# Kernel optimization log

Measured on AMD Instinct MI355X. Metric: run time of the kernel, lower is better.

The kernel has to match this reference:

```python
import jax, jax.numpy as jnp
import numpy as np

DIM = 128
P = (2, 2, 2)
D_STATE = 8
D_CONV = 4
EXPAND = 2
D_INNER = EXPAND * DIM
DT_RANK = (DIM + 15) // 16  # ceil(d_model/16) = 8
EPS = 1e-5


def setup_inputs() -> dict:
    key = jax.random.key(0)
    ks = jax.random.split(key, 8)
    B, C, Z, H, W = 2, DIM, 40, 40, 40
    s = lambda k, shape, scale: jax.random.normal(k, shape, jnp.float32) * scale
    return {
        "x": jax.random.normal(ks[0], (B, C, Z, H, W), jnp.float32),
        "norm_g": jnp.ones((C,), jnp.float32),
        "norm_b": jnp.zeros((C,), jnp.float32),
        "in_proj_w": s(ks[1], (2 * D_INNER, C), 0.02),
        "conv_w": s(ks[2], (D_INNER, D_CONV), 0.1),
        "conv_b": jnp.zeros((D_INNER,), jnp.float32),
        "x_proj_w": s(ks[3], (DT_RANK + 2 * D_STATE, D_INNER), 0.02),
        "dt_proj_w": s(ks[4], (D_INNER, DT_RANK), 0.1),
        # softplus^-1(0.01): small positive init for delta, as in mamba_ssm
        "dt_bias": jnp.log(jnp.expm1(jnp.full((D_INNER,), 0.01, jnp.float32))),
        # S4D-real init: A_log = log([1..d_state]) per channel
        "A_log": jnp.log(jnp.tile(jnp.arange(1, D_STATE + 1, dtype=jnp.float32), (D_INNER, 1))),
        "D_vec": jnp.ones((D_INNER,), jnp.float32),
        "out_proj_w": s(ks[5], (DIM, D_INNER), 0.02),
    }


def _mamba(xn, in_proj_w, conv_w, conv_b, x_proj_w, dt_proj_w, dt_bias, A_log, D_vec, out_proj_w):
    # xn: (NB, L, C)
    NB, L, _ = xn.shape
    xz = jnp.einsum('blc,ec->ble', xn, in_proj_w)          # (NB, L, 2*d_inner)
    xp, z = jnp.split(xz, 2, axis=-1)
    # causal depthwise conv1d, kernel D_CONV, truncated to L
    xpad = jnp.pad(xp, ((0, 0), (D_CONV - 1, 0), (0, 0)))
    conv = conv_b
    for k in range(D_CONV):
        conv = conv + xpad[:, k:k + L, :] * conv_w[:, k]
    u = jax.nn.silu(conv)                                  # (NB, L, d_inner)
    xdbl = jnp.einsum('bld,ed->ble', u, x_proj_w)
    dt, Bm, Cm = jnp.split(xdbl, [DT_RANK, DT_RANK + D_STATE], axis=-1)
    delta = jax.nn.softplus(jnp.einsum('blr,dr->bld', dt, dt_proj_w) + dt_bias)
    A = -jnp.exp(A_log)                                    # (d_inner, d_state)

    def step(h, inp):
        d_t, B_t, C_t, u_t = inp  # (NB,d_inner),(NB,d_state),(NB,d_state),(NB,d_inner)
        h = jnp.exp(d_t[:, :, None] * A) * h + (d_t * u_t)[:, :, None] * B_t[:, None, :]
        return h, jnp.einsum('bds,bs->bd', h, C_t)

    h0 = jnp.zeros((NB, D_INNER, D_STATE), xn.dtype)
    xs = (jnp.swapaxes(delta, 0, 1), jnp.swapaxes(Bm, 0, 1),
          jnp.swapaxes(Cm, 0, 1), jnp.swapaxes(u, 0, 1))
    _, ys = jax.lax.scan(step, h0, xs)                     # ys: (L, NB, d_inner)
    y = jnp.swapaxes(ys, 0, 1) + u * D_vec
    y = y * jax.nn.silu(z)
    return jnp.einsum('bld,cd->blc', y, out_proj_w)        # (NB, L, C)


def reference(x, norm_g, norm_b, in_proj_w, conv_w, conv_b, x_proj_w, dt_proj_w,
              dt_bias, A_log, D_vec, out_proj_w):
    B, C, Z, H, W = x.shape
    p1, p2, p3 = P
    NZ, NH, NW = Z // p1, H // p2, W // p3
    NB, L = B * p1 * p2 * p3, NZ * NH * NW
    # patch reshuffle: (B,C,Z,H,W) -> (B*p1*p2*p3, C, NZ, NH, NW)
    xd = x.reshape(B, C, NZ, p1, NH, p2, NW, p3).transpose(0, 3, 5, 7, 1, 2, 4, 6)
    xf = jnp.swapaxes(xd.reshape(NB, C, L), 1, 2)          # (NB, L, C)
    # LayerNorm over channel dim
    mu = xf.mean(-1, keepdims=True)
    var = xf.var(-1, keepdims=True)
    xn = (xf - mu) * jax.lax.rsqrt(var + EPS) * norm_g + norm_b
    yo = _mamba(xn, in_proj_w, conv_w, conv_b, x_proj_w, dt_proj_w, dt_bias,
                A_log, D_vec, out_proj_w)                  # (NB, L, C)
    # undo reshuffle
    xo = jnp.swapaxes(yo, 1, 2).reshape(B, p1, p2, p3, C, NZ, NH, NW)
    xo = xo.transpose(0, 4, 5, 1, 6, 2, 7, 3).reshape(B, C, Z, H, W)
    return xo + x
```

## Files before the change

kernel.cpp:

```cpp
#include <hip/hip_runtime.h>

#define NBATCH 16
#define LSEQ   8000
#define MROWS  128000
#define CDIM   128
#define DI     256
#define DS     8
#define DTR    8
#define NXP    24
#define NC     125
#define CL     64
#define CCL    32
#define CNCH   250

#define OFF_PB    0ull
#define OFF_XN    1024000ull
#define OFF_STA   1024000ull
#define OFF_STH   17408000ull
#define OFF_XP    33792000ull
#define OFF_XDBL  33792000ull
#define OFF_ZS    99328000ull
#define OFF_U     164864000ull
#define WS_NEEDED 230400000ull

#define P_G    0
#define P_B    128
#define P_IPW  256
#define P_CW   65792
#define P_CB   66816
#define P_XPW  67072
#define P_DTW  73216
#define P_DTB  75264
#define P_ALOG 75520
#define P_DVEC 77568
#define P_OPW  77824
#define P_TOT  110592

typedef __attribute__((ext_vector_type(8))) short bf16x8;
typedef __attribute__((ext_vector_type(4))) float f32x4;
typedef __attribute__((ext_vector_type(2))) float f32x2;

__device__ __forceinline__ float bf2f(unsigned short a) {
    union { unsigned int u; float f; } v; v.u = ((unsigned int)a) << 16; return v.f;
}
__device__ __forceinline__ unsigned short f2bf(float f) {
    union { float f; unsigned int u; } v; v.f = f;
    unsigned int r = v.u + 0x7FFFu + ((v.u >> 16) & 1u);
    return (unsigned short)(r >> 16);
}
__device__ __forceinline__ bool bfmode(const void* g) {
    return ((const unsigned int*)g)[0] == 0x3F803F80u;
}
__device__ __forceinline__ float rd(const void* p, size_t i, bool bf) {
    return bf ? bf2f(((const unsigned short*)p)[i]) : ((const float*)p)[i];
}
__device__ __forceinline__ f32x2 pk_fma(f32x2 a, f32x2 b, f32x2 c) {
    f32x2 d;
    asm("v_pk_fma_f32 %0, %1, %2, %3" : "=v"(d) : "v"(a), "v"(b), "v"(c));
    return d;
}
__device__ __forceinline__ f32x2 pk_mul(f32x2 a, f32x2 b) {
    f32x2 d;
    asm("v_pk_mul_f32 %0, %1, %2" : "=v"(d) : "v"(a), "v"(b));
    return d;
}
__device__ __forceinline__ int m_of(int b, int sp) {
    int z = sp / 1600;
    int rem = sp - z * 1600;
    int h = rem / 40;
    int w = rem - h * 40;
    int nb = b * 8 + (z & 1) * 4 + (h & 1) * 2 + (w & 1);
    int l = (z >> 1) * 400 + (h >> 1) * 20 + (w >> 1);
    return nb * LSEQ + l;
}

__global__ __launch_bounds__(256) void param_convert(const void* g, const void* b, const void* ipw,
                                                     const void* cw, const void* cb, const void* xpw,
                                                     const void* dtw, const void* dtb, const void* alog,
                                                     const void* dvec, const void* opw,
                                                     unsigned short* __restrict__ pb)
{
    int gid = blockIdx.x * 256 + threadIdx.x;
    if (gid >= P_TOT) return;
    bool bf = bfmode(g);
    const void* src; int off;
    if      (gid < P_B)    { src = g;    off = P_G; }
    else if (gid < P_IPW)  { src = b;    off = P_B; }
    else if (gid < P_CW)   { src = ipw;  off = P_IPW; }
    else if (gid < P_CB)   { src = cw;   off = P_CW; }
    else if (gid < P_XPW)  { src = cb;   off = P_CB; }
    else if (gid < P_DTW)  { src = xpw;  off = P_XPW; }
    else if (gid < P_DTB)  { src = dtw;  off = P_DTW; }
    else if (gid < P_ALOG) { src = dtb;  off = P_DTB; }
    else if (gid < P_DVEC) { src = alog; off = P_ALOG; }
    else if (gid < P_OPW)  { src = dvec; off = P_DVEC; }
    else                   { src = opw;  off = P_OPW; }
    pb[gid] = f2bf(rd(src, gid - off, bf));
}

__global__ __launch_bounds__(256) void lnorm_kernel(const void* __restrict__ x,
                                                    const unsigned short* __restrict__ pb,
                                                    unsigned short* __restrict__ xn)
{
    __shared__ float tile[128][65];
    __shared__ float psum[4][64], psqs[4][64];
    __shared__ float smu[64], srs[64];
    int b  = blockIdx.y;
    int sp0 = blockIdx.x * 64;
    int t = threadIdx.x;

    int spi = t & 63, cpart = t >> 6;
    const float* xf = (const float*)x;
#pragma unroll
    for (int pass = 0; pass < 32; ++pass) {
        int c = pass * 4 + cpart;
        tile[c][spi] = xf[((size_t)b * CDIM + c) * 64000 + sp0 + spi];
    }
    __syncthreads();

    {
        float s = 0.f, ss = 0.f;
        int c0 = cpart * 32;
#pragma unroll
        for (int cc = 0; cc < 32; ++cc) {
            float v = tile[c0 + cc][spi];
            s += v; ss += v * v;
        }
        psum[cpart][spi] = s; psqs[cpart][spi] = ss;
    }
    __syncthreads();
    if (cpart == 0) {
        float s  = psum[0][spi] + psum[1][spi] + psum[2][spi] + psum[3][spi];
        float ss = psqs[0][spi] + psqs[1][spi] + psqs[2][spi] + psqs[3][spi];
        float m = s * (1.f / CDIM);
        float var = ss * (1.f / CDIM) - m * m;
        smu[spi] = m;
        srs[spi] = rsqrtf(var + 1e-5f);
    }
    __syncthreads();

    int c = t & 127, half = t >> 7;
    float gc = bf2f(pb[P_G + c]), bc = bf2f(pb[P_B + c]);
#pragma unroll
    for (int pass = 0; pass < 32; ++pass) {
        int j = pass * 2 + half;
        int m = m_of(b, sp0 + j);
        float v = (tile[c][j] - smu[j]) * srs[j] * gc + bc;
        xn[(size_t)m * CDIM + c] = f2bf(v);
    }
}

__global__ __launch_bounds__(256) void gemm_bt_kernel(const unsigned short* __restrict__ A,
                                                      const unsigned short* __restrict__ W,
                                                      void* __restrict__ D,
                                                      int K, int Nact, int ldd, int act)
{
    __shared__ unsigned short As[128 * 32];
    __shared__ unsigned short Ws[128 * 32];
    int tid = threadIdx.x;
    int m0 = blockIdx.x * 128;
    int n0 = blockIdx.y * 128;
    int wave = tid >> 6, lane = tid & 63;
    int wm = (wave & 1) * 64, wn = (wave >> 1) * 64;
    int lrow = lane & 15, lk = (lane >> 4) * 8;
    int quad = lane >> 4;

    f32x4 acc[4][4];
#pragma unroll
    for (int i = 0; i < 4; i++)
#pragma unroll
        for (int j = 0; j < 4; j++) acc[i][j] = (f32x4){0.f, 0.f, 0.f, 0.f};

    int rowA0 = tid >> 2, kcA0 = (tid & 3) << 3;
    int rowA1 = (tid + 256) >> 2, kcA1 = (tid & 3) << 3;

    for (int kt = 0; kt < K; kt += 32) {
        *(uint4*)&As[rowA0 * 32 + kcA0] = *(const uint4*)&A[(size_t)(m0 + rowA0) * K + kt + kcA0];
        *(uint4*)&As[rowA1 * 32 + kcA1] = *(const uint4*)&A[(size_t)(m0 + rowA1) * K + kt + kcA1];
        uint4 z4 = {0u, 0u, 0u, 0u};
        uint4 w0 = (n0 + rowA0 < Nact) ? *(const uint4*)&W[(size_t)(n0 + rowA0) * K + kt + kcA0] : z4;
        uint4 w1 = (n0 + rowA1 < Nact) ? *(const uint4*)&W[(size_t)(n0 + rowA1) * K + kt + kcA1] : z4;
        *(uint4*)&Ws[rowA0 * 32 + kcA0] = w0;
        *(uint4*)&Ws[rowA1 * 32 + kcA1] = w1;
        __syncthreads();

        bf16x8 af[4], bfr[4];
#pragma unroll
        for (int i = 0; i < 4; i++) af[i]  = *(const bf16x8*)&As[(wm + i * 16 + lrow) * 32 + lk];
#pragma unroll
        for (int j = 0; j < 4; j++) bfr[j] = *(const bf16x8*)&Ws[(wn + j * 16 + lrow) * 32 + lk];
#pragma unroll
        for (int i = 0; i < 4; i++)
#pragma unroll
            for (int j = 0; j < 4; j++)
                acc[i][j] = __builtin_amdgcn_mfma_f32_16x16x32_bf16(af[i], bfr[j], acc[i][j], 0, 0, 0);
        __syncthreads();
    }

#pragma unroll
    for (int i = 0; i < 4; i++)
#pragma unroll
        for (int j = 0; j < 4; j++) {
            int n = n0 + wn + j * 16 + lrow;
            if (n < Nact) {
#pragma unroll
                for (int r = 0; r < 4; r++) {
                    int m = m0 + wm + i * 16 + quad * 4 + r;
                    float v = acc[i][j][r];
                    if (act == 2) {
                        ((float*)D)[(size_t)m * ldd + n] = v;
                    } else {
                        if (act == 1) v = v / (1.f + __expf(-v));
                        ((unsigned short*)D)[(size_t)m * ldd + n] = f2bf(v);
                    }
                }
            }
        }
}

__global__ __launch_bounds__(256) void conv_kernel(const unsigned short* __restrict__ xp,
                                                   const unsigned short* __restrict__ cw,
                                                   const unsigned short* __restrict__ cb,
                                                   unsigned short* __restrict__ u)
{
    int t = threadIdx.x;
    int oct = t & 31;
    int grp = blockIdx.x * 8 + (t >> 5);
    int nb = grp / CNCH;
    int chunk = grp - nb * CNCH;
    int l0 = chunk * CCL;
    int d0 = oct * 8;

    float w0[8], w1[8], w2[8], w3[8], bias[8];
#pragma unroll
    for (int j = 0; j < 8; j++) {
        bias[j] = bf2f(cb[d0 + j]);
        w0[j] = bf2f(cw[(d0 + j) * 4 + 0]);
        w1[j] = bf2f(cw[(d0 + j) * 4 + 1]);
        w2[j] = bf2f(cw[(d0 + j) * 4 + 2]);
        w3[j] = bf2f(cw[(d0 + j) * 4 + 3]);
    }

    size_t rowbase = (size_t)nb * LSEQ;
    bf16x8 zv;
#pragma unroll
    for (int j = 0; j < 8; j++) zv[j] = 0;
    bf16x8 xm3 = (l0 >= 3) ? *(const bf16x8*)&xp[(rowbase + l0 - 3) * DI + d0] : zv;
    bf16x8 xm2 = (l0 >= 2) ? *(const bf16x8*)&xp[(rowbase + l0 - 2) * DI + d0] : zv;
    bf16x8 xm1 = (l0 >= 1) ? *(const bf16x8*)&xp[(rowbase + l0 - 1) * DI + d0] : zv;

#pragma unroll 8
    for (int i = 0; i < CCL; ++i) {
        size_t row = rowbase + l0 + i;
        bf16x8 cur = *(const bf16x8*)&xp[row * DI + d0];
        bf16x8 res;
#pragma unroll
        for (int j = 0; j < 8; j++) {
            float acc = bias[j]
                + w0[j] * bf2f((unsigned short)xm3[j])
                + w1[j] * bf2f((unsigned short)xm2[j])
                + w2[j] * bf2f((unsigned short)xm1[j])
                + w3[j] * bf2f((unsigned short)cur[j]);
            float uv = acc / (1.f + __expf(-acc));
            res[j] = (short)f2bf(uv);
        }
        *(bf16x8*)&u[row * DI + d0] = res;
        xm3 = xm2; xm2 = xm1; xm1 = cur;
    }
}


#define BODY1(UR) do {                                                           \
    const f32x2* rq = (const f32x2*)rfp;                                         \
    f32x2 din2 = pk_mul(rq[0], Wq[0]);                                           \
    din2 = pk_fma(rq[1], Wq[1], din2);                                           \
    din2 = pk_fma(rq[2], Wq[2], din2);                                           \
    din2 = pk_fma(rq[3], Wq[3], din2);                                           \
    float din = din2.x + din2.y + bias;                                          \
    float e = __expf(din);                                                       \
    float w = 1.f + e;                                                           \
    float p1 = __builtin_amdgcn_rcpf(w);                                         \
    float delta = (din > 15.f) ? din : __logf(w);                                \
    float du = delta * bf2f(UR);                                                 \
    float p2 = p1 * p1;                                                          \
    f32x2 q1; q1.x = p1; q1.y = p2;                                              \
    f32x2 pp2; pp2.x = p2; pp2.y = p2;                                           \
    f32x2 q2 = pk_mul(q1, pp2);                                                  \
    f32x2 pp4; pp4.x = q2.y; pp4.y = q2.y;                                       \
    f32x2 q3 = pk_mul(q1, pp4);                                                  \
    f32x2 q4 = pk_mul(q2, pp4);                                                  \
    f32x2 du2; du2.x = du; du2.y = du;                                           \
    h2[0] = pk_fma(du2, rq[4], pk_mul(q1, h2[0]));                               \
    h2[1] = pk_fma(du2, rq[5], pk_mul(q2, h2[1]));                               \
    h2[2] = pk_fma(du2, rq[6], pk_mul(q3, h2[2]));                               \
    h2[3] = pk_fma(du2, rq[7], pk_mul(q4, h2[3]));                               \
    P *= p1;                                                                     \
    rfp += NXP;                                                                  \
} while (0)

__global__ __launch_bounds__(256) void scan_phase1(const unsigned short* __restrict__ u,
                                                   const float* __restrict__ xdbl,
                                                   const unsigned short* __restrict__ dtw,
                                                   const unsigned short* __restrict__ dtb,
                                                   const unsigned short* __restrict__ alog,
                                                   float* __restrict__ stA, float* __restrict__ stH)
{
    __shared__ float xs[CL * NXP];
    int c = blockIdx.x, nb = blockIdx.y, d = threadIdx.x;
    size_t base = (size_t)nb * LSEQ + (size_t)c * CL;
    {
        const uint4* src = (const uint4*)(xdbl + base * NXP);
        uint4* dst = (uint4*)xs;
        int tt = threadIdx.x;
        dst[tt] = src[tt];
        if (tt < 128) dst[256 + tt] = src[256 + tt];
    }
    float Av[DS];
    f32x2 Wq[4];
#pragma unroll
    for (int r = 0; r < 4; r++) {
        Wq[r].x = bf2f(dtw[d * DTR + 2 * r]);
        Wq[r].y = bf2f(dtw[d * DTR + 2 * r + 1]);
    }
#pragma unroll
    for (int s = 0; s < DS; s++) Av[s] = -__expf(bf2f(alog[d * DS + s]));
    float A1 = Av[0];
    bool fast = (A1 == -1.0f);
#pragma unroll
    for (int s = 1; s < DS; s++)
        fast = fast && (fabsf(Av[s] - (float)(s + 1) * A1) <= 0.02f * (float)(s + 1) * fabsf(A1));
    float bias = bf2f(dtb[d]);
    size_t o = (((size_t)c * NBATCH + nb) * DI + d) * DS;
    const unsigned short* up = u + base * DI + d;
    __syncthreads();

    if (fast) {
        f32x2 h2[4];
#pragma unroll
        for (int i = 0; i < 4; i++) { h2[i].x = 0.f; h2[i].y = 0.f; }
        float P = 1.f;
        const float* rfp = xs;
        unsigned short u0 = up[0], u1 = up[DI];
        const unsigned short* uld = up + 2 * DI;
#pragma unroll 2
        for (int t = 0; t < CL - 2; ++t) {
            unsigned short un = *uld; uld += DI;
            BODY1(u0);
            u0 = u1; u1 = un;
        }
        BODY1(u0);
        BODY1(u1);
        float P2 = P * P, P3 = P2 * P, P4 = P2 * P2;
        float apv[DS] = {P, P2, P3, P4, P4 * P, P3 * P3, P4 * P3, P4 * P4};
#pragma unroll
        for (int s = 0; s < DS; s++) stA[o + s] = apv[s];
#pragma unroll
        for (int i = 0; i < 4; i++) { stH[o + 2 * i] = h2[i].x; stH[o + 2 * i + 1] = h2[i].y; }
    } else {
        float Wdt[DTR];
#pragma unroll
        for (int r = 0; r < 4; r++) { Wdt[2 * r] = Wq[r].x; Wdt[2 * r + 1] = Wq[r].y; }
        float h[DS], ap[DS];
#pragma unroll
        for (int s = 0; s < DS; s++) { h[s] = 0.f; ap[s] = 1.f; }
        const float* rfp = xs;
        const unsigned short* uld = up;
#pragma unroll 1
        for (int t = 0; t < CL; ++t) {
            float uv = bf2f(*uld); uld += DI;
            float din = bias;
#pragma unroll
            for (int r = 0; r < DTR; r++) din += rfp[r] * Wdt[r];
            float delta = (din > 15.f) ? din : __logf(1.f + __expf(din));
            float du = delta * uv;
#pragma unroll
            for (int s = 0; s < DS; s++) {
                float dA = __expf(delta * Av[s]);
                h[s] = dA * h[s] + du * rfp[8 + s];
                ap[s] *= dA;
            }
            rfp += NXP;
        }
#pragma unroll
        for (int s = 0; s < DS; s++) { stA[o + s] = ap[s]; stH[o + s] = h[s]; }
    }
}

__global__ __launch_bounds__(256) void scan_phase2(float* __restrict__ stA, float* __restrict__ stH)
{
    size_t t = blockIdx.x * 256 + threadIdx.x;
    const size_t stride = (size_t)NBATCH * DI * DS;
    float hin = 0.f;
    size_t idx = t;
    float a[5], hl[5], an[5], hn[5];
#pragma unroll
    for (int j = 0; j < 5; ++j) { a[j] = stA[idx + j * stride]; hl[j] = stH[idx + j * stride]; }
#pragma unroll 1
    for (int g = 0; g < 25; ++g) {
        size_t nidx = idx + 5 * stride;
        if (g < 24) {
#pragma unroll
            for (int j = 0; j < 5; ++j) { an[j] = stA[nidx + j * stride]; hn[j] = stH[nidx + j * stride]; }
        }
#pragma unroll
        for (int j = 0; j < 5; ++j) {
            stH[idx + j * stride] = hin;
            hin = a[j] * hin + hl[j];
        }
#pragma unroll
        for (int j = 0; j < 5; ++j) { a[j] = an[j]; hl[j] = hn[j]; }
        idx = nidx;
    }
}

#define BODY3(UR, ZR) do {                                                       \
    const f32x2* rq = (const f32x2*)rfp;                                         \
    f32x2 din2 = pk_mul(rq[0], Wq[0]);                                           \
    din2 = pk_fma(rq[1], Wq[1], din2);                                           \
    din2 = pk_fma(rq[2], Wq[2], din2);                                           \
    din2 = pk_fma(rq[3], Wq[3], din2);                                           \
    float din = din2.x + din2.y + bias;                                          \
    float e = __expf(din);                                                       \
    float w = 1.f + e;                                                           \
    float p1 = __builtin_amdgcn_rcpf(w);                                         \
    float delta = (din > 15.f) ? din : __logf(w);                                \
    float uv = bf2f(UR);                                                         \
    float du = delta * uv;                                                       \
    float p2 = p1 * p1;                                                          \
    f32x2 q1; q1.x = p1; q1.y = p2;                                              \
    f32x2 pp2; pp2.x = p2; pp2.y = p2;                                           \
    f32x2 q2 = pk_mul(q1, pp2);                                                  \
    f32x2 pp4; pp4.x = q2.y; pp4.y = q2.y;                                       \
    f32x2 q3 = pk_mul(q1, pp4);                                                  \
    f32x2 q4 = pk_mul(q2, pp4);                                                  \
    f32x2 du2; du2.x = du; du2.y = du;                                           \
    h2[0] = pk_fma(du2, rq[4], pk_mul(q1, h2[0]));                               \
    h2[1] = pk_fma(du2, rq[5], pk_mul(q2, h2[1]));                               \
    h2[2] = pk_fma(du2, rq[6], pk_mul(q3, h2[2]));                               \
    h2[3] = pk_fma(du2, rq[7], pk_mul(q4, h2[3]));                               \
    f32x2 y2v = pk_mul(h2[0], rq[8]);                                            \
    y2v = pk_fma(h2[1], rq[9], y2v);                                             \
    y2v = pk_fma(h2[2], rq[10], y2v);                                            \
    y2v = pk_fma(h2[3], rq[11], y2v);                                            \
    float y = y2v.x + y2v.y + uv * Dv;                                           \
    *zw = f2bf(y * bf2f(ZR)); zw += DI;                                          \
    rfp += NXP;                                                                  \
} while (0)

__global__ __launch_bounds__(256) void scan_phase3(unsigned short* __restrict__ zs,
                                                   const unsigned short* __restrict__ u,
                                                   const float* __restrict__ xdbl,
                                                   const unsigned short* __restrict__ dtw,
                                                   const unsigned short* __restrict__ dtb,
                                                   const unsigned short* __restrict__ alog,
                                                   const unsigned short* __restrict__ dvec,
                                                   const float* __restrict__ stH)
{
    __shared__ float xs[CL * NXP];
    int c = blockIdx.x, nb = blockIdx.y, d = threadIdx.x;
    size_t base = (size_t)nb * LSEQ + (size_t)c * CL;
    {
        const uint4* src = (const uint4*)(xdbl + base * NXP);
        uint4* dst = (uint4*)xs;
        int tt = threadIdx.x;
        dst[tt] = src[tt];
        if (tt < 128) dst[256 + tt] = src[256 + tt];
    }
    float Av[DS];
    f32x2 Wq[4];
#pragma unroll
    for (int r = 0; r < 4; r++) {
        Wq[r].x = bf2f(dtw[d * DTR + 2 * r]);
        Wq[r].y = bf2f(dtw[d * DTR + 2 * r + 1]);
    }
#pragma unroll
    for (int s = 0; s < DS; s++) Av[s] = -__expf(bf2f(alog[d * DS + s]));
    float A1 = Av[0];
    bool fast = (A1 == -1.0f);
#pragma unroll
    for (int s = 1; s < DS; s++)
        fast = fast && (fabsf(Av[s] - (float)(s + 1) * A1) <= 0.02f * (float)(s + 1) * fabsf(A1));
    float bias = bf2f(dtb[d]);
    float Dv = bf2f(dvec[d]);
    size_t o = (((size_t)c * NBATCH + nb) * DI + d) * DS;
    const unsigned short* up = u + base * DI + d;
    unsigned short* zp = zs + base * DI + d;
    __syncthreads();

    if (fast) {
        f32x2 h2[4];
#pragma unroll
        for (int i = 0; i < 4; i++) { h2[i].x = stH[o + 2 * i]; h2[i].y = stH[o + 2 * i + 1]; }
        const float* rfp = xs;
        unsigned short u0 = up[0], u1 = up[DI];
        unsigned short z0 = zp[0], z1 = zp[DI];
        const unsigned short* uld = up + 2 * DI;
        const unsigned short* zld = zp + 2 * DI;
        unsigned short* zw = zp;
#pragma unroll 2
        for (int t = 0; t < CL - 2; ++t) {
            unsigned short un = *uld; uld += DI;
            unsigned short zn = *zld; zld += DI;
            BODY3(u0, z0);
            u0 = u1; u1 = un;
            z0 = z1; z1 = zn;
        }
        BODY3(u0, z0);
        BODY3(u1, z1);
    } else {
        float Wdt[DTR];
#pragma unroll
        for (int r = 0; r < 4; r++) { Wdt[2 * r] = Wq[r].x; Wdt[2 * r + 1] = Wq[r].y; }
        float h[DS];
#pragma unroll
        for (int s = 0; s < DS; s++) h[s] = stH[o + s];
        const float* rfp = xs;
        const unsigned short* uld = up;
        unsigned short* zw = zp;
#pragma unroll 1
        for (int t = 0; t < CL; ++t) {
            float uv = bf2f(*uld); uld += DI;
            float szv = bf2f(*zw);
            float din = bias;
#pragma unroll
            for (int r = 0; r < DTR; r++) din += rfp[r] * Wdt[r];
            float delta = (din > 15.f) ? din : __logf(1.f + __expf(din));
            float du = delta * uv;
            float y = 0.f;
#pragma unroll
            for (int s = 0; s < DS; s++) {
                float dA = __expf(delta * Av[s]);
                h[s] = dA * h[s] + du * rfp[8 + s];
                y += h[s] * rfp[16 + s];
            }
            y += uv * Dv;
            *zw = f2bf(y * szv);
            zw += DI;
            rfp += NXP;
        }
    }
}

__global__ __launch_bounds__(256) void unpatch_kernel(const void* __restrict__ x,
                                                      const unsigned short* __restrict__ y2,
                                                      float* __restrict__ out)
{
    __shared__ float ytile[64][129];
    int b  = blockIdx.y;
    int sp0 = blockIdx.x * 64;
    int t = threadIdx.x;

    {
        int c = t & 127, half = t >> 7;
#pragma unroll
        for (int pass = 0; pass < 32; ++pass) {
            int j = pass * 2 + half;
            int m = m_of(b, sp0 + j);
            ytile[j][c] = bf2f(y2[(size_t)m * CDIM + c]);
        }
    }
    __syncthreads();

    const float* xf = (const float*)x;
    int spi = t & 63, cpart = t >> 6;
#pragma unroll
    for (int pass = 0; pass < 32; ++pass) {
        int c = pass * 4 + cpart;
        size_t idx = ((size_t)b * CDIM + c) * 64000 + sp0 + spi;
        out[idx] = xf[idx] + ytile[spi][c];
    }
}

extern "C" void kernel_launch(void* const* d_in, const int* in_sizes, int n_in,
                              void* d_out, int out_size, void* d_ws, size_t ws_size,
                              hipStream_t stream)
{
    const void* x     = d_in[0];
    const void* ng    = d_in[1];
    const void* nb_   = d_in[2];
    const void* ipw   = d_in[3];
    const void* cw    = d_in[4];
    const void* cb    = d_in[5];
    const void* xpw   = d_in[6];
    const void* dtw   = d_in[7];
    const void* dtb   = d_in[8];
    const void* alog  = d_in[9];
    const void* dvec  = d_in[10];
    const void* opw   = d_in[11];
    float* out = (float*)d_out;

    if (ws_size < WS_NEEDED) return;

    char* ws = (char*)d_ws;
    unsigned short* pb   = (unsigned short*)(ws + OFF_PB);
    unsigned short* xn   = (unsigned short*)(ws + OFF_XN);
    float* stA = (float*)(ws + OFF_STA);
    float* stH = (float*)(ws + OFF_STH);
    unsigned short* xp   = (unsigned short*)(ws + OFF_XP);
    float* xdblf = (float*)(ws + OFF_XDBL);
    unsigned short* zs   = (unsigned short*)(ws + OFF_ZS);
    unsigned short* u    = (unsigned short*)(ws + OFF_U);
    unsigned short* y2   = xn;

    param_convert<<<432, 256, 0, stream>>>(ng, nb_, ipw, cw, cb, xpw, dtw, dtb, alog, dvec, opw, pb);
    lnorm_kernel<<<dim3(1000, 2), 256, 0, stream>>>(x, pb, xn);
    gemm_bt_kernel<<<dim3(1000, 2), 256, 0, stream>>>(xn, pb + P_IPW,             xp, CDIM, DI, DI, 0);
    gemm_bt_kernel<<<dim3(1000, 2), 256, 0, stream>>>(xn, pb + P_IPW + 256 * 128, zs, CDIM, DI, DI, 1);
    conv_kernel<<<500, 256, 0, stream>>>(xp, pb + P_CW, pb + P_CB, u);
    gemm_bt_kernel<<<dim3(1000, 1), 256, 0, stream>>>(u, pb + P_XPW, xdblf, DI, NXP, NXP, 2);
    scan_phase1<<<dim3(NC, NBATCH), 256, 0, stream>>>(u, xdblf, pb + P_DTW, pb + P_DTB, pb + P_ALOG,
                                                      stA, stH);
    scan_phase2<<<128, 256, 0, stream>>>(stA, stH);
    scan_phase3<<<dim3(NC, NBATCH), 256, 0, stream>>>(zs, u, xdblf, pb + P_DTW, pb + P_DTB,
                                                      pb + P_ALOG, pb + P_DVEC, stH);
    gemm_bt_kernel<<<dim3(1000, 1), 256, 0, stream>>>(zs, pb + P_OPW, y2, DI, CDIM, CDIM, 0);
    unpatch_kernel<<<dim3(1000, 2), 256, 0, stream>>>(x, y2, out);
}
```

Measured before the change: 450.4 us.

## Fuse in_proj x-half GEMM with causal conv+SiLU, vectorize scan loads

Replaces the separate xp GEMM and conv kernel with one kernel that computes a 128-row tile (with a 3-row halo) of the in_proj output into LDS, then applies the depthwise causal conv and SiLU directly, writing u. This removes the xp round trip through global memory and one launch, at the cost of recomputing the 3 halo rows per tile and a serial per-column conv loop. The scan phase bodies also switch to 128-bit LDS loads of the x_dbl row, fold the dt bias into the first packed FMA, and use hardware bf16 conversion.

```diff
diff --git a/kernel.cpp b/kernel.cpp
--- a/kernel.cpp
+++ b/kernel.cpp
@@ -10,8 +10,6 @@
 #define NXP    24
 #define NC     125
 #define CL     64
-#define CCL    32
-#define CNCH   250
 
 #define OFF_PB    0ull
 #define OFF_XN    1024000ull
@@ -47,6 +45,11 @@
     union { float f; unsigned int u; } v; v.f = f;
     unsigned int r = v.u + 0x7FFFu + ((v.u >> 16) & 1u);
     return (unsigned short)(r >> 16);
+}
+__device__ __forceinline__ unsigned short f2bf_cvt(float f) {
+    unsigned int r;
+    asm("v_cvt_pk_bf16_f32 %0, %1, %2" : "=v"(r) : "v"(f), "v"(0.f));
+    return (unsigned short)r;
 }
 __device__ __forceinline__ bool bfmode(const void* g) {
     return ((const unsigned int*)g)[0] == 0x3F803F80u;
@@ -218,65 +221,109 @@
         }
 }
 
-__global__ __launch_bounds__(256) void conv_kernel(const unsigned short* __restrict__ xp,
-                                                   const unsigned short* __restrict__ cw,
-                                                   const unsigned short* __restrict__ cb,
-                                                   unsigned short* __restrict__ u)
-{
-    int t = threadIdx.x;
-    int oct = t & 31;
-    int grp = blockIdx.x * 8 + (t >> 5);
-    int nb = grp / CNCH;
-    int chunk = grp - nb * CNCH;
-    int l0 = chunk * CCL;
-    int d0 = oct * 8;
-
-    float w0[8], w1[8], w2[8], w3[8], bias[8];
-#pragma unroll
-    for (int j = 0; j < 8; j++) {
-        bias[j] = bf2f(cb[d0 + j]);
-        w0[j] = bf2f(cw[(d0 + j) * 4 + 0]);
-        w1[j] = bf2f(cw[(d0 + j) * 4 + 1]);
-        w2[j] = bf2f(cw[(d0 + j) * 4 + 2]);
-        w3[j] = bf2f(cw[(d0 + j) * 4 + 3]);
-    }
-
-    size_t rowbase = (size_t)nb * LSEQ;
-    bf16x8 zv;
-#pragma unroll
-    for (int j = 0; j < 8; j++) zv[j] = 0;
-    bf16x8 xm3 = (l0 >= 3) ? *(const bf16x8*)&xp[(rowbase + l0 - 3) * DI + d0] : zv;
-    bf16x8 xm2 = (l0 >= 2) ? *(const bf16x8*)&xp[(rowbase + l0 - 2) * DI + d0] : zv;
-    bf16x8 xm1 = (l0 >= 1) ? *(const bf16x8*)&xp[(rowbase + l0 - 1) * DI + d0] : zv;
-
-#pragma unroll 8
-    for (int i = 0; i < CCL; ++i) {
-        size_t row = rowbase + l0 + i;
-        bf16x8 cur = *(const bf16x8*)&xp[row * DI + d0];
-        bf16x8 res;
-#pragma unroll
-        for (int j = 0; j < 8; j++) {
-            float acc = bias[j]
-                + w0[j] * bf2f((unsigned short)xm3[j])
-                + w1[j] * bf2f((unsigned short)xm2[j])
-                + w2[j] * bf2f((unsigned short)xm1[j])
-                + w3[j] * bf2f((unsigned short)cur[j]);
-            float uv = acc / (1.f + __expf(-acc));
-            res[j] = (short)f2bf(uv);
-        }
-        *(bf16x8*)&u[row * DI + d0] = res;
-        xm3 = xm2; xm2 = xm1; xm1 = cur;
-    }
-}
-
-
-#define BODY1(UR) do {                                                           \
-    const f32x2* rq = (const f32x2*)rfp;                                         \
-    f32x2 din2 = pk_mul(rq[0], Wq[0]);                                           \
-    din2 = pk_fma(rq[1], Wq[1], din2);                                           \
-    din2 = pk_fma(rq[2], Wq[2], din2);                                           \
-    din2 = pk_fma(rq[3], Wq[3], din2);                                           \
-    float din = din2.x + din2.y + bias;                                          \
+__global__ __launch_bounds__(256) void gemm_conv_kernel(const unsigned short* __restrict__ A,
+                                                        const unsigned short* __restrict__ W,
+                                                        const unsigned short* __restrict__ cw,
+                                                        const unsigned short* __restrict__ cb,
+                                                        unsigned short* __restrict__ u)
+{
+    __shared__ unsigned short As[128 * 32];
+    __shared__ unsigned short Ws[128 * 32];
+    __shared__ unsigned short Dt[128 * 132];
+
+    int tid = threadIdx.x;
+    int tile = blockIdx.x & 63;
+    int nb = blockIdx.x >> 6;
+    int n0 = blockIdx.y * 128;
+    int m0 = nb * 8000 + tile * 125;
+    int mA = m0 - 3;
+    int wave = tid >> 6, lane = tid & 63;
+    int wm = (wave & 1) * 64, wn = (wave >> 1) * 64;
+    int lrow = lane & 15, lk = (lane >> 4) * 8;
+    int quad = lane >> 4;
+
+    f32x4 acc[4][4];
+#pragma unroll
+    for (int i = 0; i < 4; i++)
+#pragma unroll
+        for (int j = 0; j < 4; j++) acc[i][j] = (f32x4){0.f, 0.f, 0.f, 0.f};
+
+    int rowA0 = tid >> 2, kcA0 = (tid & 3) << 3;
+    int rowA1 = (tid + 256) >> 2;
+
+    for (int kt = 0; kt < CDIM; kt += 32) {
+        uint4 z4 = {0u, 0u, 0u, 0u};
+        uint4 a0 = (tile == 0 && rowA0 < 3) ? z4
+                 : *(const uint4*)&A[(size_t)(mA + rowA0) * CDIM + kt + kcA0];
+        uint4 a1 = *(const uint4*)&A[(size_t)(mA + rowA1) * CDIM + kt + kcA0];
+        *(uint4*)&As[rowA0 * 32 + kcA0] = a0;
+        *(uint4*)&As[rowA1 * 32 + kcA0] = a1;
+        *(uint4*)&Ws[rowA0 * 32 + kcA0] = *(const uint4*)&W[(size_t)(n0 + rowA0) * CDIM + kt + kcA0];
+        *(uint4*)&Ws[rowA1 * 32 + kcA0] = *(const uint4*)&W[(size_t)(n0 + rowA1) * CDIM + kt + kcA0];
+        __syncthreads();
+
+        bf16x8 af[4], bfr[4];
+#pragma unroll
+        for (int i = 0; i < 4; i++) af[i]  = *(const bf16x8*)&As[(wm + i * 16 + lrow) * 32 + lk];
+#pragma unroll
+        for (int j = 0; j < 4; j++) bfr[j] = *(const bf16x8*)&Ws[(wn + j * 16 + lrow) * 32 + lk];
+#pragma unroll
+        for (int i = 0; i < 4; i++)
+#pragma unroll
+            for (int j = 0; j < 4; j++)
+                acc[i][j] = __builtin_amdgcn_mfma_f32_16x16x32_bf16(af[i], bfr[j], acc[i][j], 0, 0, 0);
+        __syncthreads();
+    }
+
+#pragma unroll
+    for (int i = 0; i < 4; i++)
+#pragma unroll
+        for (int j = 0; j < 4; j++) {
+            int nl = wn + j * 16 + lrow;
+            int tr = wm + i * 16 + quad * 4;
+            unsigned int c01, c23;
+            asm("v_cvt_pk_bf16_f32 %0, %1, %2" : "=v"(c01) : "v"(acc[i][j][0]), "v"(acc[i][j][1]));
+            asm("v_cvt_pk_bf16_f32 %0, %1, %2" : "=v"(c23) : "v"(acc[i][j][2]), "v"(acc[i][j][3]));
+            *(unsigned int*)&Dt[nl * 132 + tr]     = c01;
+            *(unsigned int*)&Dt[nl * 132 + tr + 2] = c23;
+        }
+    __syncthreads();
+
+    {
+        int nl = tid & 127, half = tid >> 7;
+        int dch = n0 + nl;
+        float cw0 = bf2f(cw[dch * 4 + 0]), cw1 = bf2f(cw[dch * 4 + 1]);
+        float cw2 = bf2f(cw[dch * 4 + 2]), cw3 = bf2f(cw[dch * 4 + 3]);
+        float cbv = bf2f(cb[dch]);
+        int tr0 = half ? 66 : 3;
+        int nsteps = half ? 62 : 63;
+        const unsigned short* col = &Dt[nl * 132];
+        float x0 = bf2f(col[tr0 - 3]), x1 = bf2f(col[tr0 - 2]), x2 = bf2f(col[tr0 - 1]);
+        unsigned short* uout = &u[(size_t)(m0 + tr0 - 3) * DI + dch];
+#pragma unroll 1
+        for (int k = 0; k < nsteps; ++k) {
+            float x3 = bf2f(col[tr0 + k]);
+            float a = cbv + cw0 * x0 + cw1 * x1 + cw2 * x2 + cw3 * x3;
+            float uv = a * __builtin_amdgcn_rcpf(1.f + __expf(-a));
+            *uout = f2bf_cvt(uv);
+            uout += DI;
+            x0 = x1; x1 = x2; x2 = x3;
+        }
+    }
+}
+
+
+#define BODY1(UR, RO) do {                                                       \
+    union { f32x4 q; f32x2 h[2]; } qa, qb, qc, qd;                               \
+    qa.q = *(const f32x4*)(rfp + (RO));                                          \
+    qb.q = *(const f32x4*)(rfp + (RO) + 4);                                      \
+    qc.q = *(const f32x4*)(rfp + (RO) + 8);                                      \
+    qd.q = *(const f32x4*)(rfp + (RO) + 12);                                     \
+    f32x2 din2 = pk_fma(qa.h[0], Wq[0], bias2);                                  \
+    din2 = pk_fma(qa.h[1], Wq[1], din2);                                         \
+    din2 = pk_fma(qb.h[0], Wq[2], din2);                                         \
+    din2 = pk_fma(qb.h[1], Wq[3], din2);                                         \
+    float din = din2.x + din2.y;                                                 \
     float e = __expf(din);                                                       \
     float w = 1.f + e;                                                           \
     float p1 = __builtin_amdgcn_rcpf(w);                                         \
@@ -290,12 +337,11 @@
     f32x2 q3 = pk_mul(q1, pp4);                                                  \
     f32x2 q4 = pk_mul(q2, pp4);                                                  \
     f32x2 du2; du2.x = du; du2.y = du;                                           \
-    h2[0] = pk_fma(du2, rq[4], pk_mul(q1, h2[0]));                               \
-    h2[1] = pk_fma(du2, rq[5], pk_mul(q2, h2[1]));                               \
-    h2[2] = pk_fma(du2, rq[6], pk_mul(q3, h2[2]));                               \
-    h2[3] = pk_fma(du2, rq[7], pk_mul(q4, h2[3]));                               \
+    h2[0] = pk_fma(du2, qc.h[0], pk_mul(q1, h2[0]));                             \
+    h2[1] = pk_fma(du2, qc.h[1], pk_mul(q2, h2[1]));                             \
+    h2[2] = pk_fma(du2, qd.h[0], pk_mul(q3, h2[2]));                             \
+    h2[3] = pk_fma(du2, qd.h[1], pk_mul(q4, h2[3]));                             \
     P *= p1;                                                                     \
-    rfp += NXP;                                                                  \
 } while (0)
 
 __global__ __launch_bounds__(256) void scan_phase1(const unsigned short* __restrict__ u,
@@ -330,6 +376,7 @@
     for (int s = 1; s < DS; s++)
         fast = fast && (fabsf(Av[s] - (float)(s + 1) * A1) <= 0.02f * (float)(s + 1) * fabsf(A1));
     float bias = bf2f(dtb[d]);
+    f32x2 bias2; bias2.x = bias; bias2.y = 0.f;
     size_t o = (((size_t)c * NBATCH + nb) * DI + d) * DS;
     const unsigned short* up = u + base * DI + d;
     __syncthreads();
@@ -342,14 +389,16 @@
         const float* rfp = xs;
         unsigned short u0 = up[0], u1 = up[DI];
         const unsigned short* uld = up + 2 * DI;
-#pragma unroll 2
-        for (int t = 0; t < CL - 2; ++t) {
-            unsigned short un = *uld; uld += DI;
-            BODY1(u0);
-            u0 = u1; u1 = un;
-        }
-        BODY1(u0);
-        BODY1(u1);
+#pragma unroll 1
+        for (int t = 0; t < CL - 2; t += 2) {
+            unsigned short ua = uld[0], ub = uld[DI]; uld += 2 * DI;
+            BODY1(u0, 0);
+            BODY1(u1, NXP);
+            u0 = ua; u1 = ub;
+            rfp += 2 * NXP;
+        }
+        BODY1(u0, 0);
+        BODY1(u1, NXP);
         float P2 = P * P, P3 = P2 * P, P4 = P2 * P2;
         float apv[DS] = {P, P2, P3, P4, P4 * P, P3 * P3, P4 * P3, P4 * P4};
 #pragma unroll
@@ -413,13 +462,19 @@
     }
 }
 
-#define BODY3(UR, ZR) do {                                                       \
-    const f32x2* rq = (const f32x2*)rfp;                                         \
-    f32x2 din2 = pk_mul(rq[0], Wq[0]);                                           \
-    din2 = pk_fma(rq[1], Wq[1], din2);                                           \
-    din2 = pk_fma(rq[2], Wq[2], din2);                                           \
-    din2 = pk_fma(rq[3], Wq[3], din2);                                           \
-    float din = din2.x + din2.y + bias;                                          \
+#define BODY3(UR, ZR, RO, ZO) do {                                               \
+    union { f32x4 q; f32x2 h[2]; } qa, qb, qc, qd, qe, qf;                       \
+    qa.q = *(const f32x4*)(rfp + (RO));                                          \
+    qb.q = *(const f32x4*)(rfp + (RO) + 4);                                      \
+    qc.q = *(const f32x4*)(rfp + (RO) + 8);                                      \
+    qd.q = *(const f32x4*)(rfp + (RO) + 12);                                     \
+    qe.q = *(const f32x4*)(rfp + (RO) + 16);                                     \
+    qf.q = *(const f32x4*)(rfp + (RO) + 20);                                     \
+    f32x2 din2 = pk_fma(qa.h[0], Wq[0], bias2);                                  \
+    din2 = pk_fma(qa.h[1], Wq[1], din2);                                         \
+    din2 = pk_fma(qb.h[0], Wq[2], din2);                                         \
+    din2 = pk_fma(qb.h[1], Wq[3], din2);                                         \
+    float din = din2.x + din2.y;                                                 \
     float e = __expf(din);                                                       \
     float w = 1.f + e;                                                           \
     float p1 = __builtin_amdgcn_rcpf(w);                                         \
@@ -434,17 +489,16 @@
     f32x2 q3 = pk_mul(q1, pp4);                                                  \
     f32x2 q4 = pk_mul(q2, pp4);                                                  \
     f32x2 du2; du2.x = du; du2.y = du;                                           \
-    h2[0] = pk_fma(du2, rq[4], pk_mul(q1, h2[0]));                               \
-    h2[1] = pk_fma(du2, rq[5], pk_mul(q2, h2[1]));                               \
-    h2[2] = pk_fma(du2, rq[6], pk_mul(q3, h2[2]));                               \
-    h2[3] = pk_fma(du2, rq[7], pk_mul(q4, h2[3]));                               \
-    f32x2 y2v = pk_mul(h2[0], rq[8]);                                            \
-    y2v = pk_fma(h2[1], rq[9], y2v);                                             \
-    y2v = pk_fma(h2[2], rq[10], y2v);                                            \
-    y2v = pk_fma(h2[3], rq[11], y2v);                                            \
-    float y = y2v.x + y2v.y + uv * Dv;                                           \
-    *zw = f2bf(y * bf2f(ZR)); zw += DI;                                          \
-    rfp += NXP;                                                                  \
+    h2[0] = pk_fma(du2, qc.h[0], pk_mul(q1, h2[0]));                             \
+    h2[1] = pk_fma(du2, qc.h[1], pk_mul(q2, h2[1]));                             \
+    h2[2] = pk_fma(du2, qd.h[0], pk_mul(q3, h2[2]));                             \
+    h2[3] = pk_fma(du2, qd.h[1], pk_mul(q4, h2[3]));                             \
+    f32x2 y2v = pk_mul(h2[0], qe.h[0]);                                          \
+    y2v = pk_fma(h2[1], qe.h[1], y2v);                                           \
+    y2v = pk_fma(h2[2], qf.h[0], y2v);                                           \
+    y2v = pk_fma(h2[3], qf.h[1], y2v);                                           \
+    float y = __builtin_fmaf(uv, Dv, y2v.x) + y2v.y;                             \
+    zw[ZO] = f2bf_cvt(y * bf2f(ZR));                                             \
 } while (0)
 
 __global__ __launch_bounds__(256) void scan_phase3(unsigned short* __restrict__ zs,
@@ -481,6 +535,7 @@
     for (int s = 1; s < DS; s++)
         fast = fast && (fabsf(Av[s] - (float)(s + 1) * A1) <= 0.02f * (float)(s + 1) * fabsf(A1));
     float bias = bf2f(dtb[d]);
+    f32x2 bias2; bias2.x = bias; bias2.y = 0.f;
     float Dv = bf2f(dvec[d]);
     size_t o = (((size_t)c * NBATCH + nb) * DI + d) * DS;
     const unsigned short* up = u + base * DI + d;
@@ -497,16 +552,17 @@
         const unsigned short* uld = up + 2 * DI;
         const unsigned short* zld = zp + 2 * DI;
         unsigned short* zw = zp;
-#pragma unroll 2
-        for (int t = 0; t < CL - 2; ++t) {
-            unsigned short un = *uld; uld += DI;
-            unsigned short zn = *zld; zld += DI;
-            BODY3(u0, z0);
-            u0 = u1; u1 = un;
-            z0 = z1; z1 = zn;
-        }
-        BODY3(u0, z0);
-        BODY3(u1, z1);
+#pragma unroll 1
+        for (int t = 0; t < CL - 2; t += 2) {
+            unsigned short ua = uld[0], ub = uld[DI]; uld += 2 * DI;
+            unsigned short za = zld[0], zb = zld[DI]; zld += 2 * DI;
+            BODY3(u0, z0, 0, 0);
+            BODY3(u1, z1, NXP, DI);
+            u0 = ua; u1 = ub; z0 = za; z1 = zb;
+            zw += 2 * DI; rfp += 2 * NXP;
+        }
+        BODY3(u0, z0, 0, 0);
+        BODY3(u1, z1, NXP, DI);
     } else {
         float Wdt[DTR];
 #pragma unroll
@@ -596,7 +652,6 @@
     unsigned short* xn   = (unsigned short*)(ws + OFF_XN);
     float* stA = (float*)(ws + OFF_STA);
     float* stH = (float*)(ws + OFF_STH);
-    unsigned short* xp   = (unsigned short*)(ws + OFF_XP);
     float* xdblf = (float*)(ws + OFF_XDBL);
     unsigned short* zs   = (unsigned short*)(ws + OFF_ZS);
     unsigned short* u    = (unsigned short*)(ws + OFF_U);
@@ -604,9 +659,8 @@
 
     param_convert<<<432, 256, 0, stream>>>(ng, nb_, ipw, cw, cb, xpw, dtw, dtb, alog, dvec, opw, pb);
     lnorm_kernel<<<dim3(1000, 2), 256, 0, stream>>>(x, pb, xn);
-    gemm_bt_kernel<<<dim3(1000, 2), 256, 0, stream>>>(xn, pb + P_IPW,             xp, CDIM, DI, DI, 0);
+    gemm_conv_kernel<<<dim3(1024, 2), 256, 0, stream>>>(xn, pb + P_IPW, pb + P_CW, pb + P_CB, u);
     gemm_bt_kernel<<<dim3(1000, 2), 256, 0, stream>>>(xn, pb + P_IPW + 256 * 128, zs, CDIM, DI, DI, 1);
-    conv_kernel<<<500, 256, 0, stream>>>(xp, pb + P_CW, pb + P_CB, u);
     gemm_bt_kernel<<<dim3(1000, 1), 256, 0, stream>>>(u, pb + P_XPW, xdblf, DI, NXP, NXP, 2);
     scan_phase1<<<dim3(NC, NBATCH), 256, 0, stream>>>(u, xdblf, pb + P_DTW, pb + P_DTB, pb + P_ALOG,
                                                       stA, stH);
```

Measured after the change: 411.1 us. 8.7% less time.
